# Kernel tuning notes

Measured on AMD Instinct MI355X. Metric: run time of the kernel, lower is better.

## Reference

```python
import jax, jax.numpy as jnp
import numpy as np
import math

B, S, E, H, DK = 2, 2048, 1024, 16, 64  # batch, seq, embed, heads, d_k (= n_wires)

def setup_inputs() -> dict:
    key = jax.random.key(0)
    k1, k2, k3, k4, k5 = jax.random.split(key, 5)
    scale = 0.02
    return {
        "x": jax.random.normal(k1, (B, S, E), dtype=jnp.float32),
        "Wk": jax.random.normal(k2, (E, E), dtype=jnp.float32) * scale,
        "Wv": jax.random.normal(k3, (E, E), dtype=jnp.float32) * scale,
        "Wq": jax.random.normal(k4, (H, DK, E), dtype=jnp.float32) * scale,
        "theta": jax.random.normal(k5, (DK,), dtype=jnp.float32) * scale,
    }

def reference(x, Wk, Wv, Wq, theta):
    batch, seq, embed = x.shape
    n_heads, d_k = Wq.shape[0], Wq.shape[1]
    # K, V projections (nn.Linear, no bias): x @ W.T
    k = (x @ Wk.T).reshape(batch, seq, n_heads, d_k).transpose(0, 2, 1, 3)  # [B,H,S,dk]
    v = (x @ Wv.T).reshape(batch, seq, n_heads, d_k).transpose(0, 2, 1, 3)  # [B,H,S,dk]
    # Quantum query path: per-head linear proj -> RX(proj_i) then RX(theta_i) on wire i from |0>,
    # MeasureAll(PauliZ) on independent wires gives <Z_i> = cos(proj_i + theta_i) exactly.
    proj = jnp.einsum('bse,hde->bhsd', x, Wq)          # [B,H,S,dk]
    q = jnp.cos(proj + theta)                           # [B,H,S,dk]
    scores = jnp.einsum('bhsd,bhtd->bhst', q, k) / math.sqrt(d_k)  # [B,H,S,S]
    attn = jax.nn.softmax(scores, axis=-1)
    out = jnp.einsum('bhst,bhtd->bhsd', attn, v)        # [B,H,S,dk]
    return out.transpose(0, 2, 1, 3).reshape(batch, seq, embed)
```

## Files before the change

kernel.cpp:

```cpp
#include <hip/hip_runtime.h>
#include <hip/hip_bf16.h>

constexpr int B  = 2;
constexpr int S  = 2048;
constexpr int E  = 1024;
constexpr int H  = 16;
constexpr int DK = 64;
constexpr int M  = B * S;
constexpr int N3 = 3 * E;
constexpr long RSZ = (long)B * H * S * DK;

#define QSCALE 0.18033688011112042f

using bf16x8 = __attribute__((ext_vector_type(8))) __bf16;
using bf16x4 = __attribute__((ext_vector_type(4))) __bf16;
using f32x4  = __attribute__((ext_vector_type(4))) float;

__device__ __forceinline__ void async16(__bf16* lds, const __bf16* g) {
    __builtin_amdgcn_global_load_lds(
        (const __attribute__((address_space(1))) void*)g,
        (__attribute__((address_space(3))) void*)lds, 16, 0, 0);
}

__global__ __launch_bounds__(256)
void cvt_kernel(const float* __restrict__ x, const float* __restrict__ Wk,
                const float* __restrict__ Wv, const float* __restrict__ Wq,
                __bf16* __restrict__ xb, __bf16* __restrict__ wall) {
    const long e = ((long)blockIdx.x * 256 + threadIdx.x) * 4;
    const float* src;
    __bf16* dst;
    if (e < (long)M * E) { src = x + e; dst = xb + e; }
    else {
        const long e2 = e - (long)M * E;
        const int which = (int)(e2 >> 20);
        const long off  = e2 & ((1L << 20) - 1);
        src = (which == 0 ? Wk : which == 1 ? Wv : Wq) + off;
        dst = wall + e2;
    }
    float4 f = *reinterpret_cast<const float4*>(src);
    bf16x4 o;
    o[0] = (__bf16)f.x; o[1] = (__bf16)f.y; o[2] = (__bf16)f.z; o[3] = (__bf16)f.w;
    *reinterpret_cast<bf16x4*>(dst) = o;
}

__global__ __launch_bounds__(256, 3)
void qkv_gemm(const __bf16* __restrict__ xb, const __bf16* __restrict__ wall,
              const float* __restrict__ theta, __bf16* __restrict__ kvq) {
    __shared__ __align__(1024) __bf16 smem[6 * 128 * 32];
    __bf16* tile = smem;

    const int t    = threadIdx.x;
    const int lane = t & 63;
    const int w    = t >> 6;
    const int quad = lane >> 4;
    const int l16  = lane & 15;
    const int wm   = w >> 1, wn = w & 1;

    const int id   = blockIdx.x;
    const int xcd  = id & 7;
    const int lid  = id >> 3;
    const int lr   = lid / 12, lc0 = lid % 12;
    const int mbase = ((xcd >> 1) * 8 + lr) * 128;
    const int nbase = ((xcd & 1) * 12 + lc0) * 128;

    f32x4 acc[4][4];
    #pragma unroll
    for (int i = 0; i < 4; i++)
        #pragma unroll
        for (int j = 0; j < 4; j++)
            acc[i][j] = f32x4{0.f, 0.f, 0.f, 0.f};

    const int srow = lane >> 2;
    const int srcc = (lane & 3) ^ ((lane >> 3) & 3);
    const __bf16* ga = xb   + (long)(mbase + srow) * E + srcc * 8;
    const __bf16* gb = wall + (long)(nbase + srow) * E + srcc * 8;

    const int csw = (l16 >> 1) & 3;

    #pragma unroll
    for (int pt = 0; pt < 2; pt++) {
        #pragma unroll
        for (int c = 0; c < 2; c++) {
            async16(smem + pt * 4096 +         (c * 64 + w * 16) * 32,
                    ga + (long)(c * 64 + w * 16) * E + pt * 32);
            async16(smem + pt * 4096 + 12288 + (c * 64 + w * 16) * 32,
                    gb + (long)(c * 64 + w * 16) * E + pt * 32);
        }
    }

    int cur = 0;
    constexpr int ITERS = E / 32;
    for (int it = 0; it < ITERS; it++) {
        if (it < ITERS - 1) asm volatile("s_waitcnt vmcnt(4)" ::: "memory");
        else                asm volatile("s_waitcnt vmcnt(0)" ::: "memory");
        asm volatile("s_barrier" ::: "memory");

        if (it + 2 < ITERS) {
            const int pb  = (cur == 0) ? 2 : cur - 1;
            const int kk2 = (it + 2) * 32;
            #pragma unroll
            for (int c = 0; c < 2; c++) {
                async16(smem + pb * 4096 +         (c * 64 + w * 16) * 32,
                        ga + (long)(c * 64 + w * 16) * E + kk2);
                async16(smem + pb * 4096 + 12288 + (c * 64 + w * 16) * 32,
                        gb + (long)(c * 64 + w * 16) * E + kk2);
            }
        }

        const __bf16* Asb = smem + cur * 4096;
        const __bf16* Bsb = smem + cur * 4096 + 12288;
        bf16x8 a[4], b[4];
        #pragma unroll
        for (int i = 0; i < 4; i++)
            a[i] = *reinterpret_cast<const bf16x8*>(
                &Asb[(wm * 64 + i * 16 + l16) * 32 + (quad ^ csw) * 8]);
        #pragma unroll
        for (int j = 0; j < 4; j++)
            b[j] = *reinterpret_cast<const bf16x8*>(
                &Bsb[(wn * 64 + j * 16 + l16) * 32 + (quad ^ csw) * 8]);
        #pragma unroll
        for (int i = 0; i < 4; i++)
            #pragma unroll
            for (int j = 0; j < 4; j++)
                acc[i][j] = __builtin_amdgcn_mfma_f32_16x16x32_bf16(a[i], b[j], acc[i][j], 0, 0, 0);

        cur = (cur == 2) ? 0 : cur + 1;
    }

    const int region = nbase >> 10;
    const int bb = mbase >> 11;
    __syncthreads();
    if (region == 1) {
        #pragma unroll
        for (int i = 0; i < 4; i++) {
            const int cchunk = wm * 8 + i * 2 + (quad >> 1);
            #pragma unroll
            for (int j = 0; j < 4; j++) {
                const int cirb = wn * 64 + j * 16 + l16;
                const int cs = cchunk ^ l16;
                bf16x4 pk;
                #pragma unroll
                for (int r = 0; r < 4; r++) pk[r] = (__bf16)acc[i][j][r];
                *reinterpret_cast<bf16x4*>(&tile[cirb * 128 + cs * 8 + (quad & 1) * 4]) = pk;
            }
        }
        __syncthreads();
        const int h0 = (nbase & 1023) >> 6;
        __bf16* vt = kvq + RSZ;
        #pragma unroll
        for (int p = 0; p < 8; p++) {
            const int dcol = p * 16 + (t >> 4);
            const int lc = t & 15;
            const int cs2 = lc ^ (dcol & 15);
            bf16x8 vv = *reinterpret_cast<const bf16x8*>(&tile[dcol * 128 + cs2 * 8]);
            const int hh = h0 + (dcol >> 6), d = dcol & 63;
            *reinterpret_cast<bf16x8*>(
                &vt[((long)(bb * H + hh) * DK + d) * S + (mbase & 2047) + lc * 8]) = vv;
        }
    } else {
        __bf16* dst = kvq + (region == 2 ? 2 * RSZ : 0);
        float th[4];
        if (region == 2) {
            #pragma unroll
            for (int j = 0; j < 4; j++) th[j] = theta[j * 16 + l16];
        }
        #pragma unroll
        for (int i = 0; i < 4; i++) {
            #pragma unroll
            for (int j = 0; j < 4; j++) {
                const int c = wn * 64 + j * 16 + l16;
                #pragma unroll
                for (int r = 0; r < 4; r++) {
                    const int cir = wm * 64 + i * 16 + quad * 4 + r;
                    float v = acc[i][j][r];
                    if (region == 2) v = cosf(v + th[j]) * QSCALE;
                    tile[cir * 132 + c] = (__bf16)v;
                }
            }
        }
        __syncthreads();
        const int h0 = (nbase & 1023) >> 6;
        #pragma unroll
        for (int p = 0; p < 8; p++) {
            const int row = p * 16 + (t >> 4);
            const int lc  = t & 15;
            bf16x8 vv = *reinterpret_cast<const bf16x8*>(&tile[row * 132 + lc * 8]);
            const int s = (mbase + row) & 2047;
            const int h = h0 + (lc >> 3), d = (lc & 7) * 8;
            *reinterpret_cast<bf16x8*>(
                &dst[((long)(bb * H + h) * S + s) * DK + d]) = vv;
        }
    }
}

__global__ __launch_bounds__(256, 2)
void attn_kernel(const __bf16* __restrict__ q_ws, const __bf16* __restrict__ k_ws,
                 const __bf16* __restrict__ v_ws, float* __restrict__ out) {
    __shared__ __align__(1024) __bf16 Ks[3][64 * 64];
    __shared__ __align__(1024) __bf16 Vs[3][64 * 64];
    __shared__ __align__(16)   __bf16 Pl[4][32 * 72];
    __shared__ __align__(16)   float  ls_lds[4][32];

    const int lane = threadIdx.x & 63;
    const int w    = threadIdx.x >> 6;
    const int quad = lane >> 4;
    const int l16  = lane & 15;

    const int id    = blockIdx.x;
    const int bh    = (id & 7) + 8 * ((id >> 3) & 3);
    const int qbase = (id >> 5) * 128 + w * 32;

    const __bf16* qp = q_ws + (long)bh * S * DK;
    const __bf16* kp = k_ws + (long)bh * S * DK;
    const __bf16* vp = v_ws + (long)bh * DK * S;

    const int sr  = lane >> 3;
    const int scs = (lane & 7) ^ sr;

    bf16x8 bq[2][2];
    #pragma unroll
    for (int nt = 0; nt < 2; nt++)
        #pragma unroll
        for (int ks = 0; ks < 2; ks++)
            bq[nt][ks] = *reinterpret_cast<const bf16x8*>(
                qp + (long)(qbase + nt * 16 + l16) * DK + ks * 32 + quad * 8);

    f32x4 o[2][4];
    #pragma unroll
    for (int i = 0; i < 2; i++)
        #pragma unroll
        for (int j = 0; j < 4; j++) o[i][j] = f32x4{0.f, 0.f, 0.f, 0.f};
    float lsum[2] = {0.f, 0.f};

    #pragma unroll
    for (int pt = 0; pt < 2; pt++) {
        #pragma unroll
        for (int i = 0; i < 2; i++) {
            const int row = w * 16 + i * 8;
            async16(&Ks[pt][row * 64], kp + (long)(pt * 64 + row + sr) * DK + scs * 8);
            async16(&Vs[pt][row * 64], vp + (long)(row + sr) * S + pt * 64 + scs * 8);
        }
    }

    int cur = 0;
    constexpr int ITERS = S / 64;
    for (int it = 0; it < ITERS; it++) {
        if (it < ITERS - 1) asm volatile("s_waitcnt vmcnt(4)" ::: "memory");
        else                asm volatile("s_waitcnt vmcnt(0)" ::: "memory");
        asm volatile("s_barrier" ::: "memory");

        if (it + 2 < ITERS) {
            const int kt2 = (it + 2) * 64;
            const int pb  = (cur == 0) ? 2 : cur - 1;
            #pragma unroll
            for (int i = 0; i < 2; i++) {
                const int row = w * 16 + i * 8;
                async16(&Ks[pb][row * 64], kp + (long)(kt2 + row + sr) * DK + scs * 8);
                async16(&Vs[pb][row * 64], vp + (long)(row + sr) * S + kt2 + scs * 8);
            }
        }

        f32x4 sacc[4][2];
        #pragma unroll
        for (int i = 0; i < 4; i++)
            #pragma unroll
            for (int j = 0; j < 2; j++) sacc[i][j] = f32x4{0.f, 0.f, 0.f, 0.f};
        #pragma unroll
        for (int ks = 0; ks < 2; ks++) {
            bf16x8 ak[4];
            #pragma unroll
            for (int mt = 0; mt < 4; mt++)
                ak[mt] = *reinterpret_cast<const bf16x8*>(
                    &Ks[cur][(mt * 16 + l16) * 64 + ((ks * 4 + quad) ^ (l16 & 7)) * 8]);
            #pragma unroll
            for (int mt = 0; mt < 4; mt++)
                #pragma unroll
                for (int nt = 0; nt < 2; nt++)
                    sacc[mt][nt] = __builtin_amdgcn_mfma_f32_16x16x32_bf16(
                        ak[mt], bq[nt][ks], sacc[mt][nt], 0, 0, 0);
        }

        #pragma unroll
        for (int mt = 0; mt < 4; mt++)
            #pragma unroll
            for (int nt = 0; nt < 2; nt++) {
                float p0 = __builtin_amdgcn_exp2f(sacc[mt][nt][0]);
                float p1 = __builtin_amdgcn_exp2f(sacc[mt][nt][1]);
                float p2 = __builtin_amdgcn_exp2f(sacc[mt][nt][2]);
                float p3 = __builtin_amdgcn_exp2f(sacc[mt][nt][3]);
                lsum[nt] += (p0 + p1) + (p2 + p3);
                bf16x4 pk;
                pk[0] = (__bf16)p0; pk[1] = (__bf16)p1;
                pk[2] = (__bf16)p2; pk[3] = (__bf16)p3;
                *reinterpret_cast<bf16x4*>(
                    &Pl[w][(nt * 16 + l16) * 72 + mt * 16 + quad * 4]) = pk;
            }

        #pragma unroll
        for (int kh = 0; kh < 2; kh++) {
            bf16x8 bv[4];
            #pragma unroll
            for (int nt = 0; nt < 4; nt++)
                bv[nt] = *reinterpret_cast<const bf16x8*>(
                    &Vs[cur][(nt * 16 + l16) * 64 + ((kh * 4 + quad) ^ (l16 & 7)) * 8]);
            #pragma unroll
            for (int mt = 0; mt < 2; mt++) {
                bf16x8 ap = *reinterpret_cast<const bf16x8*>(
                    &Pl[w][(mt * 16 + l16) * 72 + kh * 32 + quad * 8]);
                #pragma unroll
                for (int nt = 0; nt < 4; nt++)
                    o[mt][nt] = __builtin_amdgcn_mfma_f32_16x16x32_bf16(
                        ap, bv[nt], o[mt][nt], 0, 0, 0);
            }
        }

        cur = (cur == 2) ? 0 : cur + 1;
    }

    #pragma unroll
    for (int nt = 0; nt < 2; nt++) {
        float v = lsum[nt];
        v += __shfl_xor(v, 16);
        v += __shfl_xor(v, 32);
        ls_lds[w][nt * 16 + l16] = v;
    }

    __syncthreads();
    float* scr = (w < 3) ? (float*)&Ks[w][0] : (float*)&Vs[0][0];
    const int b = bh >> 4, h = bh & 15;
    #pragma unroll
    for (int mt = 0; mt < 2; mt++) {
        f32x4 lv = *reinterpret_cast<const f32x4*>(&ls_lds[w][mt * 16 + quad * 4]);
        #pragma unroll
        for (int r = 0; r < 4; r++) {
            const float inv = 1.0f / lv[r];
            const int row = mt * 16 + quad * 4 + r;
            #pragma unroll
            for (int nt = 0; nt < 4; nt++)
                scr[row * 64 + nt * 16 + l16] = o[mt][nt][r] * inv;
        }
    }
    __syncthreads();
    #pragma unroll
    for (int p = 0; p < 8; p++) {
        const int c = p * 64 + lane;
        const int row = c >> 4, chunk = c & 15;
        f32x4 v4 = *reinterpret_cast<const f32x4*>(&scr[row * 64 + chunk * 4]);
        const int srow = qbase + row;
        *reinterpret_cast<f32x4*>(
            &out[(long)(b * S + srow) * E + h * DK + chunk * 4]) = v4;
    }
}

extern "C" void kernel_launch(void* const* d_in, const int* in_sizes, int n_in,
                              void* d_out, int out_size, void* d_ws, size_t ws_size,
                              hipStream_t stream) {
    const float* x     = (const float*)d_in[0];
    const float* Wk    = (const float*)d_in[1];
    const float* Wv    = (const float*)d_in[2];
    const float* Wq    = (const float*)d_in[3];
    const float* theta = (const float*)d_in[4];
    float* out = (float*)d_out;

    __bf16* kvq  = (__bf16*)d_ws;
    __bf16* k_ws = kvq;
    __bf16* v_t  = kvq + RSZ;
    __bf16* q_ws = kvq + 2 * RSZ;
    __bf16* xb   = (__bf16*)d_out;
    __bf16* wall = xb + (long)M * E;

    dim3 blk(256);
    cvt_kernel<<<dim3(7168), blk, 0, stream>>>(x, Wk, Wv, Wq, xb, wall);
    qkv_gemm<<<dim3(768), blk, 0, stream>>>(xb, wall, theta, kvq);
    attn_kernel<<<dim3(512), blk, 0, stream>>>(q_ws, k_ws, v_t, out);
}
```

Measured before the change: 169.5 us.

## Fuse fp32-to-bf16 conversion into QKV GEMM, loading fp32 tiles directly

Removes the separate conversion kernel and has the QKV GEMM stream fp32 x and weight tiles into LDS asynchronously, converting to bf16 in registers just before the MFMAs. This drops one launch plus the write and re-read of the bf16 copies of x and all weights. In exchange, LDS and global traffic per tile doubles because the tiles are fp32, the pipeline shrinks from three buffers to two with a full vmcnt(0) wait every step, and occupancy is lowered to 2 blocks per SM. Each weight tile is also converted again by every block that reads it.

```diff
diff --git a/kernel.cpp b/kernel.cpp
--- a/kernel.cpp
+++ b/kernel.cpp
@@ -21,33 +21,27 @@
         (const __attribute__((address_space(1))) void*)g,
         (__attribute__((address_space(3))) void*)lds, 16, 0, 0);
 }
-
-__global__ __launch_bounds__(256)
-void cvt_kernel(const float* __restrict__ x, const float* __restrict__ Wk,
-                const float* __restrict__ Wv, const float* __restrict__ Wq,
-                __bf16* __restrict__ xb, __bf16* __restrict__ wall) {
-    const long e = ((long)blockIdx.x * 256 + threadIdx.x) * 4;
-    const float* src;
-    __bf16* dst;
-    if (e < (long)M * E) { src = x + e; dst = xb + e; }
-    else {
-        const long e2 = e - (long)M * E;
-        const int which = (int)(e2 >> 20);
-        const long off  = e2 & ((1L << 20) - 1);
-        src = (which == 0 ? Wk : which == 1 ? Wv : Wq) + off;
-        dst = wall + e2;
-    }
-    float4 f = *reinterpret_cast<const float4*>(src);
-    bf16x4 o;
-    o[0] = (__bf16)f.x; o[1] = (__bf16)f.y; o[2] = (__bf16)f.z; o[3] = (__bf16)f.w;
-    *reinterpret_cast<bf16x4*>(dst) = o;
-}
-
-__global__ __launch_bounds__(256, 3)
-void qkv_gemm(const __bf16* __restrict__ xb, const __bf16* __restrict__ wall,
-              const float* __restrict__ theta, __bf16* __restrict__ kvq) {
-    __shared__ __align__(1024) __bf16 smem[6 * 128 * 32];
-    __bf16* tile = smem;
+__device__ __forceinline__ void async16f(float* lds, const float* g) {
+    __builtin_amdgcn_global_load_lds(
+        (const __attribute__((address_space(1))) void*)g,
+        (__attribute__((address_space(3))) void*)lds, 16, 0, 0);
+}
+
+__device__ __forceinline__ bf16x8 cvt8(f32x4 lo, f32x4 hi) {
+    bf16x8 r;
+    r[0] = (__bf16)lo[0]; r[1] = (__bf16)lo[1];
+    r[2] = (__bf16)lo[2]; r[3] = (__bf16)lo[3];
+    r[4] = (__bf16)hi[0]; r[5] = (__bf16)hi[1];
+    r[6] = (__bf16)hi[2]; r[7] = (__bf16)hi[3];
+    return r;
+}
+
+__global__ __launch_bounds__(256, 2)
+void qkv_fused(const float* __restrict__ x, const float* __restrict__ Wk,
+               const float* __restrict__ Wv, const float* __restrict__ Wq,
+               const float* __restrict__ theta, __bf16* __restrict__ kvq) {
+    __shared__ __align__(1024) float smemf[4 * 4096];
+    __bf16* tile = (__bf16*)smemf;
 
     const int t    = threadIdx.x;
     const int lane = t & 63;
@@ -63,6 +57,10 @@
     const int mbase = ((xcd >> 1) * 8 + lr) * 128;
     const int nbase = ((xcd & 1) * 12 + lc0) * 128;
 
+    const int region = nbase >> 10;
+    const float* wsel = region == 0 ? Wk : region == 1 ? Wv : Wq;
+    const int nbw = nbase & 1023;
+
     f32x4 acc[4][4];
     #pragma unroll
     for (int i = 0; i < 4; i++)
@@ -70,64 +68,61 @@
         for (int j = 0; j < 4; j++)
             acc[i][j] = f32x4{0.f, 0.f, 0.f, 0.f};
 
-    const int srow = lane >> 2;
-    const int srcc = (lane & 3) ^ ((lane >> 3) & 3);
-    const __bf16* ga = xb   + (long)(mbase + srow) * E + srcc * 8;
-    const __bf16* gb = wall + (long)(nbase + srow) * E + srcc * 8;
-
-    const int csw = (l16 >> 1) & 3;
-
-    #pragma unroll
-    for (int pt = 0; pt < 2; pt++) {
-        #pragma unroll
-        for (int c = 0; c < 2; c++) {
-            async16(smem + pt * 4096 +         (c * 64 + w * 16) * 32,
-                    ga + (long)(c * 64 + w * 16) * E + pt * 32);
-            async16(smem + pt * 4096 + 12288 + (c * 64 + w * 16) * 32,
-                    gb + (long)(c * 64 + w * 16) * E + pt * 32);
-        }
-    }
-
+    const int sr  = lane >> 3;
+    const int scs = (lane & 7) ^ sr;
+
+    auto stage = [&](int buf, int kk) {
+        #pragma unroll
+        for (int i = 0; i < 4; i++) {
+            const int rb = w * 32 + i * 8;
+            async16f(smemf + buf * 4096 + rb * 32,
+                     x + (long)(mbase + rb + sr) * E + kk + scs * 4);
+            async16f(smemf + 8192 + buf * 4096 + rb * 32,
+                     wsel + (long)(nbw + rb + sr) * E + kk + scs * 4);
+        }
+    };
+
+    stage(0, 0);
+
+    const int sw8 = l16 & 7;
     int cur = 0;
     constexpr int ITERS = E / 32;
     for (int it = 0; it < ITERS; it++) {
-        if (it < ITERS - 1) asm volatile("s_waitcnt vmcnt(4)" ::: "memory");
-        else                asm volatile("s_waitcnt vmcnt(0)" ::: "memory");
+        asm volatile("s_waitcnt vmcnt(0)" ::: "memory");
         asm volatile("s_barrier" ::: "memory");
 
-        if (it + 2 < ITERS) {
-            const int pb  = (cur == 0) ? 2 : cur - 1;
-            const int kk2 = (it + 2) * 32;
-            #pragma unroll
-            for (int c = 0; c < 2; c++) {
-                async16(smem + pb * 4096 +         (c * 64 + w * 16) * 32,
-                        ga + (long)(c * 64 + w * 16) * E + kk2);
-                async16(smem + pb * 4096 + 12288 + (c * 64 + w * 16) * 32,
-                        gb + (long)(c * 64 + w * 16) * E + kk2);
-            }
-        }
-
-        const __bf16* Asb = smem + cur * 4096;
-        const __bf16* Bsb = smem + cur * 4096 + 12288;
+        if (it + 1 < ITERS) stage(cur ^ 1, (it + 1) * 32);
+
+        const float* Af = smemf + cur * 4096;
+        const float* Bf = smemf + 8192 + cur * 4096;
         bf16x8 a[4], b[4];
         #pragma unroll
-        for (int i = 0; i < 4; i++)
-            a[i] = *reinterpret_cast<const bf16x8*>(
-                &Asb[(wm * 64 + i * 16 + l16) * 32 + (quad ^ csw) * 8]);
-        #pragma unroll
-        for (int j = 0; j < 4; j++)
-            b[j] = *reinterpret_cast<const bf16x8*>(
-                &Bsb[(wn * 64 + j * 16 + l16) * 32 + (quad ^ csw) * 8]);
+        for (int i = 0; i < 4; i++) {
+            const int row = wm * 64 + i * 16 + l16;
+            f32x4 lo = *reinterpret_cast<const f32x4*>(
+                &Af[row * 32 + (((2 * quad) ^ sw8) * 4)]);
+            f32x4 hi = *reinterpret_cast<const f32x4*>(
+                &Af[row * 32 + (((2 * quad + 1) ^ sw8) * 4)]);
+            a[i] = cvt8(lo, hi);
+        }
+        #pragma unroll
+        for (int j = 0; j < 4; j++) {
+            const int row = wn * 64 + j * 16 + l16;
+            f32x4 lo = *reinterpret_cast<const f32x4*>(
+                &Bf[row * 32 + (((2 * quad) ^ sw8) * 4)]);
+            f32x4 hi = *reinterpret_cast<const f32x4*>(
+                &Bf[row * 32 + (((2 * quad + 1) ^ sw8) * 4)]);
+            b[j] = cvt8(lo, hi);
+        }
         #pragma unroll
         for (int i = 0; i < 4; i++)
             #pragma unroll
             for (int j = 0; j < 4; j++)
                 acc[i][j] = __builtin_amdgcn_mfma_f32_16x16x32_bf16(a[i], b[j], acc[i][j], 0, 0, 0);
 
-        cur = (cur == 2) ? 0 : cur + 1;
-    }
-
-    const int region = nbase >> 10;
+        cur ^= 1;
+    }
+
     const int bb = mbase >> 11;
     __syncthreads();
     if (region == 1) {
@@ -145,7 +140,7 @@
             }
         }
         __syncthreads();
-        const int h0 = (nbase & 1023) >> 6;
+        const int h0 = nbw >> 6;
         __bf16* vt = kvq + RSZ;
         #pragma unroll
         for (int p = 0; p < 8; p++) {
@@ -179,7 +174,7 @@
             }
         }
         __syncthreads();
-        const int h0 = (nbase & 1023) >> 6;
+        const int h0 = nbw >> 6;
         #pragma unroll
         for (int p = 0; p < 8; p++) {
             const int row = p * 16 + (t >> 4);
@@ -366,11 +361,8 @@
     __bf16* k_ws = kvq;
     __bf16* v_t  = kvq + RSZ;
     __bf16* q_ws = kvq + 2 * RSZ;
-    __bf16* xb   = (__bf16*)d_out;
-    __bf16* wall = xb + (long)M * E;
 
     dim3 blk(256);
-    cvt_kernel<<<dim3(7168), blk, 0, stream>>>(x, Wk, Wv, Wq, xb, wall);
-    qkv_gemm<<<dim3(768), blk, 0, stream>>>(xb, wall, theta, kvq);
+    qkv_fused<<<dim3(768), blk, 0, stream>>>(x, Wk, Wv, Wq, theta, kvq);
     attn_kernel<<<dim3(512), blk, 0, stream>>>(q_ws, k_ws, v_t, out);
 }
```

Result: slower. 185.0 us (+9.1%).
